# Kernel tuning notes

Hardware: AMD Instinct MI355X
Metric: run time of the kernel (lower is better)

The kernel has to match this reference:

```python
import jax, jax.numpy as jnp
import numpy as np

D_MODEL = 1024
NHEAD = 16
D_K = D_MODEL // NHEAD


def setup_inputs() -> dict:
    key = jax.random.key(0)
    ks = jax.random.split(key, 11)
    B, S = 4, 2048
    s = 1.0 / np.sqrt(D_MODEL)
    return {
        "query": jax.random.normal(ks[0], (B, S, D_MODEL), jnp.float32),
        "key": jax.random.normal(ks[1], (B, S, D_MODEL), jnp.float32),
        "value": jax.random.normal(ks[2], (B, S, D_MODEL), jnp.float32),
        "Wq": jax.random.normal(ks[3], (D_MODEL, D_MODEL), jnp.float32) * s,
        "bq": jnp.zeros((D_MODEL,), jnp.float32),
        "Wk": jax.random.normal(ks[4], (D_MODEL, D_MODEL), jnp.float32) * s,
        "bk": jnp.zeros((D_MODEL,), jnp.float32),
        "Wv": jax.random.normal(ks[5], (D_MODEL, D_MODEL), jnp.float32) * s,
        "bv": jnp.zeros((D_MODEL,), jnp.float32),
        "Wo": jax.random.normal(ks[6], (D_MODEL, D_MODEL), jnp.float32) * s,
        "bo": jnp.zeros((D_MODEL,), jnp.float32),
    }


def _split_heads(x):
    # [B, S, D] -> [B, H, S, d_k]
    B, S, _ = x.shape
    return x.reshape(B, S, NHEAD, D_K).transpose(0, 2, 1, 3)


def reference(query, key, value, Wq, bq, Wk, bk, Wv, bv, Wo, bo):
    # torch Linear: x @ W.T + b
    q = _split_heads(query @ Wq.T + bq)
    k = _split_heads(key @ Wk.T + bk)
    v = _split_heads(value @ Wv.T + bv)
    scale = 1.0 / np.sqrt(D_K).astype(np.float32)
    scores = jnp.einsum("bhqd,bhkd->bhqk", q, k) * scale
    attn = jax.nn.softmax(scores, axis=-1)  # dropout p=0 -> identity
    out = jnp.einsum("bhqk,bhkd->bhqd", attn, v)
    B, H, S, dk = out.shape
    out = out.transpose(0, 2, 1, 3).reshape(B, S, H * dk)
    return out @ Wo.T + bo
```

## Files before the change

kernel.cpp:

```cpp
#include <hip/hip_runtime.h>
#include <stdint.h>

#define DEVI static __device__ __forceinline__

typedef __attribute__((ext_vector_type(4))) float f32x4;
typedef __attribute__((ext_vector_type(16))) float f32x16;
typedef __attribute__((ext_vector_type(8))) __bf16 bf16x8;
typedef __attribute__((ext_vector_type(4))) uint16_t u16x4;
typedef uint16_t u16;

DEVI u16 f2bf(float f) {
  union { float f; uint32_t u; } v; v.f = f;
  uint32_t r = v.u + 0x7FFFu + ((v.u >> 16) & 1u);
  return (u16)(r >> 16);
}

DEVI f32x4 mfma16(bf16x8 a, bf16x8 b, f32x4 c) {
  return __builtin_amdgcn_mfma_f32_16x16x32_bf16(a, b, c, 0, 0, 0);
}

DEVI f32x16 mfma32(bf16x8 a, bf16x8 b, f32x16 c) {
  return __builtin_amdgcn_mfma_f32_32x32x16_bf16(a, b, c, 0, 0, 0);
}

DEVI void load_lds16(const void* g, void* l) {
  __builtin_amdgcn_global_load_lds(
      (const __attribute__((address_space(1))) void*)g,
      (__attribute__((address_space(3))) void*)l, 16, 0, 0);
}

DEVI bf16x8 lds_frag(const u16* p) { return *(const bf16x8*)p; }

DEVI f32x16 zero16() {
  f32x16 z;
#pragma unroll
  for (int i = 0; i < 16; ++i) z[i] = 0.f;
  return z;
}

DEVI float exp2_hw(float x) {
  float r;
  asm("v_exp_f32 %0, %1" : "=v"(r) : "v"(x));
  return r;
}

DEVI uint32_t cvtpk(float lo, float hi) {
  uint32_t r;
  asm("v_cvt_pk_bf16_f32 %0, %1, %2" : "=v"(r) : "v"(lo), "v"(hi));
  return r;
}

DEVI float max3f(float a, float b, float c) {
  float r;
  asm("v_max3_f32 %0, %1, %2, %3" : "=v"(r) : "v"(a), "v"(b), "v"(c));
  return r;
}

DEVI float partner_f(float x) { return __shfl_xor(x, 32, 64); }

DEVI void pswap_asm(uint32_t& a, uint32_t& b) {
  asm("v_permlane32_swap_b32 %0, %1" : "+v"(a), "+v"(b));
}

#define NBIG (4 * 2048 * 1024)
#define NW (1024 * 1024)

__global__ __launch_bounds__(256) void cvt_kernel(
    const float* q, const float* k, const float* v, const float* Wq,
    const float* Wk, const float* Wv, const float* Wo, u16* qb, u16* kb,
    u16* vb, u16* Wqb, u16* Wkb, u16* Wvb, u16* Wob) {
  const float* src;
  u16* dst;
  int n;
  switch (blockIdx.y) {
    case 0: src = q;  dst = qb;  n = NBIG; break;
    case 1: src = k;  dst = kb;  n = NBIG; break;
    case 2: src = v;  dst = vb;  n = NBIG; break;
    case 3: src = Wq; dst = Wqb; n = NW;   break;
    case 4: src = Wk; dst = Wkb; n = NW;   break;
    case 5: src = Wv; dst = Wvb; n = NW;   break;
    default: src = Wo; dst = Wob; n = NW;  break;
  }
  int i = (blockIdx.x * 256 + threadIdx.x) * 4;
  if (i >= n) return;
  float4 f = *(const float4*)&src[i];
  u16x4 o;
  o.x = f2bf(f.x); o.y = f2bf(f.y); o.z = f2bf(f.z); o.w = f2bf(f.w);
  *(u16x4*)&dst[i] = o;
}

DEVI void gemm_core_1024_db(const u16* __restrict__ A,
                            const u16* __restrict__ Bm, int bm, int bn,
                            u16* As, u16* Bs, f32x4 acc[4][4]) {
  const int tid = threadIdx.x;
  const int w = tid >> 6, l = tid & 63;
  const int lr = l & 15, lg = l >> 4;
  const int wr = (w >> 1) * 64, wc = (w & 1) * 64;

  for (int i = 0; i < 4; ++i)
    for (int j = 0; j < 4; ++j) acc[i][j] = (f32x4){0.f, 0.f, 0.f, 0.f};

  const int c0 = 2 * w, c1 = 2 * w + 1;
  const u16* gA0 = A + (size_t)(bm * 128 + c0 * 16 + (l >> 2)) * 1024 + (l & 3) * 8;
  const u16* gA1 = A + (size_t)(bm * 128 + c1 * 16 + (l >> 2)) * 1024 + (l & 3) * 8;
  const u16* gB0 = Bm + (size_t)(bn * 128 + c0 * 16 + (l >> 2)) * 1024 + (l & 3) * 8;
  const u16* gB1 = Bm + (size_t)(bn * 128 + c1 * 16 + (l >> 2)) * 1024 + (l & 3) * 8;
  const int sA0 = c0 * 512, sA1 = c1 * 512;

  int aoff[4], boff[4];
#pragma unroll
  for (int mi = 0; mi < 4; ++mi) aoff[mi] = (wr + mi * 16 + lr) * 32 + lg * 8;
#pragma unroll
  for (int nj = 0; nj < 4; ++nj) boff[nj] = (wc + nj * 16 + lr) * 32 + lg * 8;

  load_lds16(gA0, As + sA0);
  load_lds16(gA1, As + sA1);
  load_lds16(gB0, Bs + sA0);
  load_lds16(gB1, Bs + sA1);
  __syncthreads();

  int cur = 0;
  for (int k0 = 0; k0 < 1024; k0 += 32) {
    const int nxt = cur ^ 1;
    if (k0 + 32 < 1024) {
      load_lds16(gA0 + k0 + 32, As + nxt * 4096 + sA0);
      load_lds16(gA1 + k0 + 32, As + nxt * 4096 + sA1);
      load_lds16(gB0 + k0 + 32, Bs + nxt * 4096 + sA0);
      load_lds16(gB1 + k0 + 32, Bs + nxt * 4096 + sA1);
    }
    const u16* Ac = As + cur * 4096;
    const u16* Bc = Bs + cur * 4096;
    bf16x8 af[4], bff[4];
#pragma unroll
    for (int mi = 0; mi < 4; ++mi) af[mi] = lds_frag(&Ac[aoff[mi]]);
#pragma unroll
    for (int nj = 0; nj < 4; ++nj) bff[nj] = lds_frag(&Bc[boff[nj]]);
#pragma unroll
    for (int mi = 0; mi < 4; ++mi)
#pragma unroll
      for (int nj = 0; nj < 4; ++nj)
        acc[mi][nj] = mfma16(af[mi], bff[nj], acc[mi][nj]);
    __syncthreads();
    cur = nxt;
  }
}

__global__ __launch_bounds__(256) void proj_kernel(
    const u16* qb, const u16* kb, const u16* vb, const u16* Wq, const u16* Wk,
    const u16* Wv, const float* bq, const float* bk, const float* bv, u16* Qp,
    u16* Kp, u16* Vt) {
  __shared__ __align__(16) u16 As[2 * 128 * 32];
  __shared__ __align__(16) u16 Bs[2 * 128 * 32];
  const int z = blockIdx.z;
  const u16* A = z == 0 ? qb : z == 1 ? kb : vb;
  const u16* W = z == 0 ? Wq : z == 1 ? Wk : Wv;
  const float* bias = z == 0 ? bq : z == 1 ? bk : bv;

  f32x4 acc[4][4];
  gemm_core_1024_db(A, W, blockIdx.x, blockIdx.y, As, Bs, acc);

  const int tid = threadIdx.x;
  const int w = tid >> 6, l = tid & 63;
  const int lr = l & 15, lg = l >> 4;
  const int wr = (w >> 1) * 64, wc = (w & 1) * 64;
  const int b = (blockIdx.x * 128) >> 11;

#pragma unroll
  for (int nj = 0; nj < 4; ++nj) {
    const int col = blockIdx.y * 128 + wc + nj * 16 + lr;
    const float bb = bias[col];
    const int h = col >> 6, d = col & 63;
#pragma unroll
    for (int mi = 0; mi < 4; ++mi) {
      const int m0 = blockIdx.x * 128 + wr + mi * 16 + lg * 4;
      const int s0 = m0 & 2047;
      if (z < 2) {
        u16* dst = (z == 0) ? Qp : Kp;
#pragma unroll
        for (int r = 0; r < 4; ++r)
          dst[(((size_t)(b * 16 + h) * 2048) + s0 + r) * 64 + d] =
              f2bf(acc[mi][nj][r] + bb);
      } else {
        u16x4 pk;
        pk.x = f2bf(acc[mi][nj][0] + bb);
        pk.y = f2bf(acc[mi][nj][1] + bb);
        pk.z = f2bf(acc[mi][nj][2] + bb);
        pk.w = f2bf(acc[mi][nj][3] + bb);
        *(u16x4*)&Vt[(((size_t)(b * 16 + h) * 64) + d) * 2048 + s0] = pk;
      }
    }
  }
}

__global__ __launch_bounds__(256) void outproj_kernel(const u16* O,
                                                      const u16* Wo,
                                                      const float* bo,
                                                      float* out) {
  __shared__ __align__(16) u16 As[2 * 128 * 32];
  __shared__ __align__(16) u16 Bs[2 * 128 * 32];
  f32x4 acc[4][4];
  gemm_core_1024_db(O, Wo, blockIdx.x, blockIdx.y, As, Bs, acc);

  const int tid = threadIdx.x;
  const int w = tid >> 6, l = tid & 63;
  const int lr = l & 15, lg = l >> 4;
  const int wr = (w >> 1) * 64, wc = (w & 1) * 64;
#pragma unroll
  for (int nj = 0; nj < 4; ++nj) {
    const int col = blockIdx.y * 128 + wc + nj * 16 + lr;
    const float bb = bo[col];
#pragma unroll
    for (int mi = 0; mi < 4; ++mi) {
      const int m0 = blockIdx.x * 128 + wr + mi * 16 + lg * 4;
#pragma unroll
      for (int r = 0; r < 4; ++r)
        out[(size_t)(m0 + r) * 1024 + col] = acc[mi][nj][r] + bb;
    }
  }
}

#define LDPK 72
#define NT 32
__global__ __launch_bounds__(512) void attn_kernel(const u16* Qp, const u16* Kp,
                                                   const u16* Vt, u16* Ob) {
  __shared__ __align__(16) u16 Kl[2][64 * LDPK];
  __shared__ __align__(16) u16 Vl[2][64 * LDPK];

  const int tid = threadIdx.x, w = tid >> 6, l = tid & 63;
  const int q = l & 31, hi = l >> 5;
  const int bh = blockIdx.y;
  const int q0 = blockIdx.x * 256 + w * 32;
  const u16* Qh = Qp + (size_t)bh * 2048 * 64;
  const u16* Kh = Kp + (size_t)bh * 2048 * 64;
  const u16* Vh = Vt + (size_t)bh * 64 * 2048;

  const float SC2 = 0.1803368801f;

  bf16x8 qf[4];
#pragma unroll
  for (int ds = 0; ds < 4; ++ds)
    qf[ds] = *(const bf16x8*)&Qh[(size_t)(q0 + q) * 64 + ds * 16 + hi * 8];

  f32x16 o0 = zero16(), o1 = zero16();
  float m = -1.0e30f, ln = 0.f;

  const int srow = tid >> 3, g0 = tid & 7;

  int koff[2][4], voff[2][4];
#pragma unroll
  for (int kb = 0; kb < 2; ++kb)
#pragma unroll
    for (int ds = 0; ds < 4; ++ds)
      koff[kb][ds] = (kb * 32 + q) * LDPK + ds * 16 + hi * 8;
#pragma unroll
  for (int db = 0; db < 2; ++db)
#pragma unroll
    for (int ks = 0; ks < 4; ++ks)
      voff[db][ks] = (db * 32 + q) * LDPK + ks * 16 + hi * 8;

  bf16x8 kv = *(const bf16x8*)&Kh[srow * 64 + g0 * 8];
  bf16x8 vv = *(const bf16x8*)&Vh[(size_t)srow * 2048 + g0 * 8];
  *(bf16x8*)&Kl[0][srow * LDPK + g0 * 8] = kv;
  *(bf16x8*)&Vl[0][srow * LDPK + g0 * 8] = vv;
  kv = *(const bf16x8*)&Kh[4096 + srow * 64 + g0 * 8];
  vv = *(const bf16x8*)&Vh[(size_t)srow * 2048 + 64 + g0 * 8];
  const u16* gk = Kh + 2 * 4096 + srow * 64 + g0 * 8;
  const u16* gv = Vh + (size_t)srow * 2048 + 2 * 64 + g0 * 8;
  __syncthreads();

  for (int kt = 0; kt < NT; ++kt) {
    const int cur = kt & 1;
    const u16* Kc = Kl[cur];
    const u16* Vc = Vl[cur];

    f32x16 c0 = zero16(), c1 = zero16();
    __builtin_amdgcn_s_setprio(1);
#pragma unroll
    for (int ds = 0; ds < 4; ++ds)
      c0 = mfma32(lds_frag(&Kc[koff[0][ds]]), qf[ds], c0);
#pragma unroll
    for (int ds = 0; ds < 4; ++ds)
      c1 = mfma32(lds_frag(&Kc[koff[1][ds]]), qf[ds], c1);
    __builtin_amdgcn_s_setprio(0);

    float tm[16];
#pragma unroll
    for (int r = 0; r < 16; ++r) tm[r] = fmaxf(c0[r], c1[r]);
    {
      const float m0_ = max3f(tm[0], tm[1], tm[2]);
      const float m1_ = max3f(tm[3], tm[4], tm[5]);
      const float m2_ = max3f(tm[6], tm[7], tm[8]);
      const float m3_ = max3f(tm[9], tm[10], tm[11]);
      const float m4_ = max3f(tm[12], tm[13], tm[14]);
      const float a_ = max3f(m0_, m1_, m2_);
      const float b_ = max3f(m3_, m4_, tm[15]);
      tm[0] = fmaxf(a_, b_);
    }
    const float mx = fmaxf(tm[0], partner_f(tm[0]));
    if (!__all(mx - m <= 64.0f)) {
      const float mnew = fmaxf(m, mx);
      const float a = exp2_hw((m - mnew) * SC2);
      m = mnew;
#pragma unroll
      for (int r = 0; r < 16; ++r) { o0[r] *= a; o1[r] *= a; }
      ln *= a;
    }
    const float m2 = m * SC2;
    float p0[16], p1[16];
#pragma unroll
    for (int r = 0; r < 16; ++r) {
      p0[r] = exp2_hw(__builtin_fmaf(c0[r], SC2, -m2));
      p1[r] = exp2_hw(__builtin_fmaf(c1[r], SC2, -m2));
    }
    float ts[16];
#pragma unroll
    for (int r = 0; r < 16; ++r) ts[r] = p0[r] + p1[r];
#pragma unroll
    for (int s = 8; s > 0; s >>= 1)
#pragma unroll
      for (int r = 0; r < s; ++r) ts[r] += ts[r + s];
    ln += ts[0] + partner_f(ts[0]);

    if (kt + 1 < NT) {
      *(bf16x8*)&Kl[cur ^ 1][srow * LDPK + g0 * 8] = kv;
      *(bf16x8*)&Vl[cur ^ 1][srow * LDPK + g0 * 8] = vv;
    }
    if (kt + 2 < NT) {
      kv = *(const bf16x8*)gk;
      vv = *(const bf16x8*)gv;
      gk += 4096; gv += 64;
    }

    uint32_t wv[16];
#pragma unroll
    for (int i = 0; i < 8; ++i) {
      wv[i]     = cvtpk(p0[2 * i], p0[2 * i + 1]);
      wv[8 + i] = cvtpk(p1[2 * i], p1[2 * i + 1]);
    }
    bf16x8 pa[4];
#pragma unroll
    for (int ks = 0; ks < 4; ++ks) {
      const int base = (ks >> 1) * 8 + 4 * (ks & 1);
      uint32_t x0 = wv[base],     y0 = wv[base + 2];
      uint32_t x1 = wv[base + 1], y1 = wv[base + 3];
      pswap_asm(x0, y0);
      pswap_asm(x1, y1);
      union { uint32_t u[4]; bf16x8 v; } cvt;
      cvt.u[0] = x0; cvt.u[1] = x1; cvt.u[2] = y0; cvt.u[3] = y1;
      pa[ks] = cvt.v;
    }

    __builtin_amdgcn_s_setprio(1);
#pragma unroll
    for (int ks = 0; ks < 4; ++ks)
      o0 = mfma32(lds_frag(&Vc[voff[0][ks]]), pa[ks], o0);
#pragma unroll
    for (int ks = 0; ks < 4; ++ks)
      o1 = mfma32(lds_frag(&Vc[voff[1][ks]]), pa[ks], o1);
    __builtin_amdgcn_s_setprio(0);

    __syncthreads();
  }

  const int b2 = bh >> 4, h = bh & 15;
  const float inv = 1.0f / ln;
  u16* orow = Ob + ((size_t)(b2 * 2048 + q0 + q)) * 1024 + h * 64;
#pragma unroll
  for (int g = 0; g < 4; ++g) {
    u16x4 pk;
    pk.x = f2bf(o0[4 * g + 0] * inv);
    pk.y = f2bf(o0[4 * g + 1] * inv);
    pk.z = f2bf(o0[4 * g + 2] * inv);
    pk.w = f2bf(o0[4 * g + 3] * inv);
    *(u16x4*)&orow[8 * g + 4 * hi] = pk;
  }
#pragma unroll
  for (int g = 0; g < 4; ++g) {
    u16x4 pk;
    pk.x = f2bf(o1[4 * g + 0] * inv);
    pk.y = f2bf(o1[4 * g + 1] * inv);
    pk.z = f2bf(o1[4 * g + 2] * inv);
    pk.w = f2bf(o1[4 * g + 3] * inv);
    *(u16x4*)&orow[32 + 8 * g + 4 * hi] = pk;
  }
}

extern "C" void kernel_launch(void* const* d_in, const int* in_sizes, int n_in,
                              void* d_out, int out_size, void* d_ws,
                              size_t ws_size, hipStream_t stream) {
  const float* q  = (const float*)d_in[0];
  const float* k  = (const float*)d_in[1];
  const float* v  = (const float*)d_in[2];
  const float* Wq = (const float*)d_in[3];
  const float* bq = (const float*)d_in[4];
  const float* Wk = (const float*)d_in[5];
  const float* bk = (const float*)d_in[6];
  const float* Wv = (const float*)d_in[7];
  const float* bv = (const float*)d_in[8];
  const float* Wo = (const float*)d_in[9];
  const float* bo = (const float*)d_in[10];
  float* out = (float*)d_out;

  u16* ws = (u16*)d_ws;
  u16* qb  = ws;
  u16* kb  = qb + NBIG;
  u16* vb  = kb + NBIG;
  u16* Wqb = vb + NBIG;
  u16* Wkb = Wqb + NW;
  u16* Wvb = Wkb + NW;
  u16* Wob = Wvb + NW;
  u16* Qp  = Wob + NW;
  u16* Kp  = Qp + NBIG;
  u16* Vt  = Kp + NBIG;
  u16* O   = qb;

  cvt_kernel<<<dim3(8192, 7, 1), 256, 0, stream>>>(q, k, v, Wq, Wk, Wv, Wo, qb,
                                                   kb, vb, Wqb, Wkb, Wvb, Wob);
  proj_kernel<<<dim3(64, 8, 3), 256, 0, stream>>>(qb, kb, vb, Wqb, Wkb, Wvb,
                                                  bq, bk, bv, Qp, Kp, Vt);
  attn_kernel<<<dim3(8, 64, 1), 512, 0, stream>>>(Qp, Kp, Vt, O);
  outproj_kernel<<<dim3(64, 8, 1), 256, 0, stream>>>(O, Wob, bo, out);
}
```

Baseline: 226.3 us.

## Use three-stage LDS pipeline with vmcnt waits in projection GEMM core

Replaces the double-buffered GEMM mainloop with a triple-buffered one that keeps two K-tiles of global-to-LDS loads in flight. It waits with s_waitcnt vmcnt(4) plus a raw s_barrier instead of __syncthreads, so the wave waits only for the oldest stage rather than draining all loads. This is meant to hide global load latency behind MFMA work in the projection and output-projection GEMMs. The cost is 50% more LDS per block, which may lower occupancy, and it relies on the exact vmcnt accounting of the load_lds16 instructions being correct.

```diff
diff --git a/kernel.cpp b/kernel.cpp
--- a/kernel.cpp
+++ b/kernel.cpp
@@ -61,6 +61,9 @@
 DEVI void pswap_asm(uint32_t& a, uint32_t& b) {
   asm("v_permlane32_swap_b32 %0, %1" : "+v"(a), "+v"(b));
 }
+
+DEVI void wait_vm4() { asm volatile("s_waitcnt vmcnt(4)" ::: "memory"); }
+DEVI void wait_vm0() { asm volatile("s_waitcnt vmcnt(0)" ::: "memory"); }
 
 #define NBIG (4 * 2048 * 1024)
 #define NW (1024 * 1024)
@@ -89,7 +92,7 @@
   *(u16x4*)&dst[i] = o;
 }
 
-DEVI void gemm_core_1024_db(const u16* __restrict__ A,
+DEVI void gemm_core_1024_p2(const u16* __restrict__ A,
                             const u16* __restrict__ Bm, int bm, int bn,
                             u16* As, u16* Bs, f32x4 acc[4][4]) {
   const int tid = threadIdx.x;
@@ -117,16 +120,25 @@
   load_lds16(gA1, As + sA1);
   load_lds16(gB0, Bs + sA0);
   load_lds16(gB1, Bs + sA1);
-  __syncthreads();
+  load_lds16(gA0 + 32, As + 4096 + sA0);
+  load_lds16(gA1 + 32, As + 4096 + sA1);
+  load_lds16(gB0 + 32, Bs + 4096 + sA0);
+  load_lds16(gB1 + 32, Bs + 4096 + sA1);
+  wait_vm4();
+  __builtin_amdgcn_sched_barrier(0);
+  __builtin_amdgcn_s_barrier();
 
   int cur = 0;
-  for (int k0 = 0; k0 < 1024; k0 += 32) {
-    const int nxt = cur ^ 1;
-    if (k0 + 32 < 1024) {
-      load_lds16(gA0 + k0 + 32, As + nxt * 4096 + sA0);
-      load_lds16(gA1 + k0 + 32, As + nxt * 4096 + sA1);
-      load_lds16(gB0 + k0 + 32, Bs + nxt * 4096 + sA0);
-      load_lds16(gB1 + k0 + 32, Bs + nxt * 4096 + sA1);
+  for (int t = 0; t < 32; ++t) {
+    if (t + 2 < 32) {
+      const int st = cur >= 1 ? cur - 1 : 2;
+      const int ko = (t + 2) * 32;
+      u16* Ab = As + st * 4096;
+      u16* Bb = Bs + st * 4096;
+      load_lds16(gA0 + ko, Ab + sA0);
+      load_lds16(gA1 + ko, Ab + sA1);
+      load_lds16(gB0 + ko, Bb + sA0);
+      load_lds16(gB1 + ko, Bb + sA1);
     }
     const u16* Ac = As + cur * 4096;
     const u16* Bc = Bs + cur * 4096;
@@ -140,8 +152,16 @@
 #pragma unroll
       for (int nj = 0; nj < 4; ++nj)
         acc[mi][nj] = mfma16(af[mi], bff[nj], acc[mi][nj]);
-    __syncthreads();
-    cur = nxt;
+    if (t + 2 < 32) {
+      wait_vm4();
+      __builtin_amdgcn_sched_barrier(0);
+      __builtin_amdgcn_s_barrier();
+    } else if (t + 1 < 32) {
+      wait_vm0();
+      __builtin_amdgcn_sched_barrier(0);
+      __builtin_amdgcn_s_barrier();
+    }
+    cur = cur == 2 ? 0 : cur + 1;
   }
 }
 
@@ -149,15 +169,15 @@
     const u16* qb, const u16* kb, const u16* vb, const u16* Wq, const u16* Wk,
     const u16* Wv, const float* bq, const float* bk, const float* bv, u16* Qp,
     u16* Kp, u16* Vt) {
-  __shared__ __align__(16) u16 As[2 * 128 * 32];
-  __shared__ __align__(16) u16 Bs[2 * 128 * 32];
+  __shared__ __align__(16) u16 As[3 * 128 * 32];
+  __shared__ __align__(16) u16 Bs[3 * 128 * 32];
   const int z = blockIdx.z;
   const u16* A = z == 0 ? qb : z == 1 ? kb : vb;
   const u16* W = z == 0 ? Wq : z == 1 ? Wk : Wv;
   const float* bias = z == 0 ? bq : z == 1 ? bk : bv;
 
   f32x4 acc[4][4];
-  gemm_core_1024_db(A, W, blockIdx.x, blockIdx.y, As, Bs, acc);
+  gemm_core_1024_p2(A, W, blockIdx.x, blockIdx.y, As, Bs, acc);
 
   const int tid = threadIdx.x;
   const int w = tid >> 6, l = tid & 63;
@@ -196,10 +216,10 @@
                                                       const u16* Wo,
                                                       const float* bo,
                                                       float* out) {
-  __shared__ __align__(16) u16 As[2 * 128 * 32];
-  __shared__ __align__(16) u16 Bs[2 * 128 * 32];
+  __shared__ __align__(16) u16 As[3 * 128 * 32];
+  __shared__ __align__(16) u16 Bs[3 * 128 * 32];
   f32x4 acc[4][4];
-  gemm_core_1024_db(O, Wo, blockIdx.x, blockIdx.y, As, Bs, acc);
+  gemm_core_1024_p2(O, Wo, blockIdx.x, blockIdx.y, As, Bs, acc);
 
   const int tid = threadIdx.x;
   const int w = tid >> 6, l = tid & 63;
```

Measured after the change: 240.9 us. +6.5%, slower.

## Rewrite QKV projection GEMM with 256x256 tiles, 512 threads, swizzled LDS pipeline

Applied to the files above, without the earlier changes.

Replaces the 128x128 projection GEMM with a 256x256-tile kernel using 8 waves, each computing 128x64. It uses K-step 64, XOR-swizzled LDS layout, and double-buffered direct-to-LDS loads staggered across four sub-phases with explicit waitcnt/barriers and setprio around MFMA bursts. This aims to raise arithmetic intensity and overlap global loads with MFMA. The trade-offs are a 384-block grid that may underfill waves on 256 CUs, higher register and LDS use, and fragile hand-tuned synchronization.

```diff
diff --git a/kernel.cpp b/kernel.cpp
--- a/kernel.cpp
+++ b/kernel.cpp
@@ -89,6 +89,149 @@
   *(u16x4*)&dst[i] = o;
 }
 
+__global__ __launch_bounds__(512) void proj_kernel(
+    const u16* qb, const u16* kb, const u16* vb, const u16* Wq, const u16* Wk,
+    const u16* Wv, const float* bq, const float* bk, const float* bv, u16* Qp,
+    u16* Kp, u16* Vt) {
+  __shared__ __align__(16) u16 As[2][2][8192];
+  __shared__ __align__(16) u16 Bs[2][2][8192];
+
+  const int z = blockIdx.z;
+  const u16* A = z == 0 ? qb : z == 1 ? kb : vb;
+  const u16* W = z == 0 ? Wq : z == 1 ? Wk : Wv;
+  const float* bias = z == 0 ? bq : z == 1 ? bk : bv;
+
+  const int tid = threadIdx.x, w = tid >> 6, l = tid & 63;
+  const int lr = l & 15, lg = l >> 4;
+  const int wm = w >> 2, wn = w & 3;
+  const int bm = blockIdx.x, bn = blockIdx.y;
+
+  const int r0 = tid >> 3;
+  const int jg = (tid & 7) ^ (r0 & 7);
+  const int r1 = r0 + 64;
+  const u16* gA0 = A + (size_t)(bm * 256 + r0) * 1024 + jg * 8;
+  const u16* gA1 = A + (size_t)(bm * 256 + r1) * 1024 + jg * 8;
+  const u16* gB0 = W + (size_t)(bn * 256 + r0) * 1024 + jg * 8;
+  const u16* gB1 = W + (size_t)(bn * 256 + r1) * 1024 + jg * 8;
+  const int ls0 = w * 512;
+  const int ls1 = 4096 + w * 512;
+
+  auto stB = [&](int dd, int h, int kt) {
+    load_lds16(gB0 + (size_t)h * 128 * 1024 + kt * 64, &Bs[dd][h][ls0]);
+    load_lds16(gB1 + (size_t)h * 128 * 1024 + kt * 64, &Bs[dd][h][ls1]);
+  };
+  auto stA_s0 = [&](int dd, int kt) {
+    load_lds16(gA0 + kt * 64, &As[dd][0][ls0]);
+    load_lds16(gA0 + (size_t)128 * 1024 + kt * 64, &As[dd][1][ls0]);
+  };
+  auto stA_s1 = [&](int dd, int kt) {
+    load_lds16(gA1 + kt * 64, &As[dd][0][ls1]);
+    load_lds16(gA1 + (size_t)128 * 1024 + kt * 64, &As[dd][1][ls1]);
+  };
+
+  int aoff[8][2], boff[4][2];
+#pragma unroll
+  for (int mi = 0; mi < 8; ++mi)
+#pragma unroll
+    for (int ks = 0; ks < 2; ++ks)
+      aoff[mi][ks] = (mi * 16 + lr) * 64 + (((ks * 4 + lg) ^ (lr & 7)) * 8);
+#pragma unroll
+  for (int nf = 0; nf < 4; ++nf)
+#pragma unroll
+    for (int ks = 0; ks < 2; ++ks)
+      boff[nf][ks] =
+          ((wn & 1) * 64 + nf * 16 + lr) * 64 + (((ks * 4 + lg) ^ (lr & 7)) * 8);
+
+  f32x4 acc[8][4];
+#pragma unroll
+  for (int i = 0; i < 8; ++i)
+#pragma unroll
+    for (int j = 0; j < 4; ++j) acc[i][j] = (f32x4){0.f, 0.f, 0.f, 0.f};
+
+  stB(0, 0, 0);
+  stB(0, 1, 0);
+  stA_s0(0, 0);
+  stA_s1(0, 0);
+  asm volatile("s_waitcnt vmcnt(2)" ::: "memory");
+  __builtin_amdgcn_sched_barrier(0);
+  __builtin_amdgcn_s_barrier();
+
+  for (int t = 0; t < 16; ++t) {
+    const int d = t & 1;
+    const u16* Aw = &As[d][wm][0];
+    const u16* Bw = &Bs[d][wn >> 1][0];
+    bf16x8 bf[4][2];
+#pragma unroll
+    for (int q = 0; q < 4; ++q) {
+      if (q == 0) {
+#pragma unroll
+        for (int nf = 0; nf < 4; ++nf)
+#pragma unroll
+          for (int ks = 0; ks < 2; ++ks)
+            bf[nf][ks] = lds_frag(&Bw[boff[nf][ks]]);
+      }
+      bf16x8 af[2][2];
+#pragma unroll
+      for (int j = 0; j < 2; ++j)
+#pragma unroll
+        for (int ks = 0; ks < 2; ++ks)
+          af[j][ks] = lds_frag(&Aw[aoff[2 * q + j][ks]]);
+      if (t + 1 < 16) {
+        if (q == 0) stB(d ^ 1, 0, t + 1);
+        else if (q == 1) stB(d ^ 1, 1, t + 1);
+        else if (q == 2) stA_s0(d ^ 1, t + 1);
+        else stA_s1(d ^ 1, t + 1);
+      }
+      __builtin_amdgcn_s_barrier();
+      asm volatile("s_waitcnt lgkmcnt(0)" ::: "memory");
+      __builtin_amdgcn_sched_barrier(0);
+      __builtin_amdgcn_s_setprio(1);
+#pragma unroll
+      for (int j = 0; j < 2; ++j)
+#pragma unroll
+        for (int ks = 0; ks < 2; ++ks)
+#pragma unroll
+          for (int nf = 0; nf < 4; ++nf)
+            acc[2 * q + j][nf] = mfma16(af[j][ks], bf[nf][ks], acc[2 * q + j][nf]);
+      __builtin_amdgcn_s_setprio(0);
+      if (q == 1) {
+        if (t < 15) asm volatile("s_waitcnt vmcnt(4)" ::: "memory");
+        else        asm volatile("s_waitcnt vmcnt(0)" ::: "memory");
+      } else if (q == 3 && t < 15) {
+        asm volatile("s_waitcnt vmcnt(2)" ::: "memory");
+      }
+      __builtin_amdgcn_s_barrier();
+    }
+  }
+
+  const int b = (bm * 256) >> 11;
+#pragma unroll
+  for (int nj = 0; nj < 4; ++nj) {
+    const int col = bn * 256 + wn * 64 + nj * 16 + lr;
+    const float bb = bias[col];
+    const int h = col >> 6, dd = col & 63;
+#pragma unroll
+    for (int mi = 0; mi < 8; ++mi) {
+      const int m0 = bm * 256 + wm * 128 + mi * 16 + lg * 4;
+      const int s0 = m0 & 2047;
+      if (z < 2) {
+        u16* dst = (z == 0) ? Qp : Kp;
+#pragma unroll
+        for (int r = 0; r < 4; ++r)
+          dst[(((size_t)(b * 16 + h) * 2048) + s0 + r) * 64 + dd] =
+              f2bf(acc[mi][nj][r] + bb);
+      } else {
+        u16x4 pk;
+        pk.x = f2bf(acc[mi][nj][0] + bb);
+        pk.y = f2bf(acc[mi][nj][1] + bb);
+        pk.z = f2bf(acc[mi][nj][2] + bb);
+        pk.w = f2bf(acc[mi][nj][3] + bb);
+        *(u16x4*)&Vt[(((size_t)(b * 16 + h) * 64) + dd) * 2048 + s0] = pk;
+      }
+    }
+  }
+}
+
 DEVI void gemm_core_1024_db(const u16* __restrict__ A,
                             const u16* __restrict__ Bm, int bm, int bn,
                             u16* As, u16* Bs, f32x4 acc[4][4]) {
@@ -142,53 +285,6 @@
         acc[mi][nj] = mfma16(af[mi], bff[nj], acc[mi][nj]);
     __syncthreads();
     cur = nxt;
-  }
-}
-
-__global__ __launch_bounds__(256) void proj_kernel(
-    const u16* qb, const u16* kb, const u16* vb, const u16* Wq, const u16* Wk,
-    const u16* Wv, const float* bq, const float* bk, const float* bv, u16* Qp,
-    u16* Kp, u16* Vt) {
-  __shared__ __align__(16) u16 As[2 * 128 * 32];
-  __shared__ __align__(16) u16 Bs[2 * 128 * 32];
-  const int z = blockIdx.z;
-  const u16* A = z == 0 ? qb : z == 1 ? kb : vb;
-  const u16* W = z == 0 ? Wq : z == 1 ? Wk : Wv;
-  const float* bias = z == 0 ? bq : z == 1 ? bk : bv;
-
-  f32x4 acc[4][4];
-  gemm_core_1024_db(A, W, blockIdx.x, blockIdx.y, As, Bs, acc);
-
-  const int tid = threadIdx.x;
-  const int w = tid >> 6, l = tid & 63;
-  const int lr = l & 15, lg = l >> 4;
-  const int wr = (w >> 1) * 64, wc = (w & 1) * 64;
-  const int b = (blockIdx.x * 128) >> 11;
-
-#pragma unroll
-  for (int nj = 0; nj < 4; ++nj) {
-    const int col = blockIdx.y * 128 + wc + nj * 16 + lr;
-    const float bb = bias[col];
-    const int h = col >> 6, d = col & 63;
-#pragma unroll
-    for (int mi = 0; mi < 4; ++mi) {
-      const int m0 = blockIdx.x * 128 + wr + mi * 16 + lg * 4;
-      const int s0 = m0 & 2047;
-      if (z < 2) {
-        u16* dst = (z == 0) ? Qp : Kp;
-#pragma unroll
-        for (int r = 0; r < 4; ++r)
-          dst[(((size_t)(b * 16 + h) * 2048) + s0 + r) * 64 + d] =
-              f2bf(acc[mi][nj][r] + bb);
-      } else {
-        u16x4 pk;
-        pk.x = f2bf(acc[mi][nj][0] + bb);
-        pk.y = f2bf(acc[mi][nj][1] + bb);
-        pk.z = f2bf(acc[mi][nj][2] + bb);
-        pk.w = f2bf(acc[mi][nj][3] + bb);
-        *(u16x4*)&Vt[(((size_t)(b * 16 + h) * 64) + d) * 2048 + s0] = pk;
-      }
-    }
   }
 }
 
@@ -416,7 +512,7 @@
 
   cvt_kernel<<<dim3(8192, 7, 1), 256, 0, stream>>>(q, k, v, Wq, Wk, Wv, Wo, qb,
                                                    kb, vb, Wqb, Wkb, Wvb, Wob);
-  proj_kernel<<<dim3(64, 8, 3), 256, 0, stream>>>(qb, kb, vb, Wqb, Wkb, Wvb,
+  proj_kernel<<<dim3(32, 4, 3), 512, 0, stream>>>(qb, kb, vb, Wqb, Wkb, Wvb,
                                                   bq, bk, bv, Qp, Kp, Vt);
   attn_kernel<<<dim3(8, 64, 1), 512, 0, stream>>>(Qp, Kp, Vt, O);
   outproj_kernel<<<dim3(64, 8, 1), 256, 0, stream>>>(O, Wob, bo, out);
```

Result: no change. 226.0 us (-0.1%).

## Fuse fp32-to-bf16 activation conversion into projection GEMM A-tile loads

Applied to the files above, without the earlier changes.

The separate conversion pass over the q/k/v activations is removed. The projection kernel now streams fp32 activations straight into LDS through an XOR-swizzled layout and converts them to bf16 in registers before the MFMA. This avoids writing and re-reading about 50 MB of bf16 intermediates and drops most of the conversion kernel's work. In exchange the A tile takes twice the LDS space and global traffic per tile, and every tile is converted again for each of the 8 column blocks.

```diff
diff --git a/kernel.cpp b/kernel.cpp
--- a/kernel.cpp
+++ b/kernel.cpp
@@ -50,6 +50,15 @@
   return r;
 }
 
+DEVI bf16x8 cvt8v(f32x4 lo, f32x4 hi) {
+  union { uint32_t u[4]; bf16x8 v; } c;
+  c.u[0] = cvtpk(lo[0], lo[1]);
+  c.u[1] = cvtpk(lo[2], lo[3]);
+  c.u[2] = cvtpk(hi[0], hi[1]);
+  c.u[3] = cvtpk(hi[2], hi[3]);
+  return c.v;
+}
+
 DEVI float max3f(float a, float b, float c) {
   float r;
   asm("v_max3_f32 %0, %1, %2, %3" : "=v"(r) : "v"(a), "v"(b), "v"(c));
@@ -65,74 +74,102 @@
 #define NBIG (4 * 2048 * 1024)
 #define NW (1024 * 1024)
 
-__global__ __launch_bounds__(256) void cvt_kernel(
-    const float* q, const float* k, const float* v, const float* Wq,
-    const float* Wk, const float* Wv, const float* Wo, u16* qb, u16* kb,
-    u16* vb, u16* Wqb, u16* Wkb, u16* Wvb, u16* Wob) {
+__global__ __launch_bounds__(256) void cvt_kernel(const float* Wq,
+                                                  const float* Wk,
+                                                  const float* Wv,
+                                                  const float* Wo, u16* Wqb,
+                                                  u16* Wkb, u16* Wvb,
+                                                  u16* Wob) {
   const float* src;
   u16* dst;
-  int n;
   switch (blockIdx.y) {
-    case 0: src = q;  dst = qb;  n = NBIG; break;
-    case 1: src = k;  dst = kb;  n = NBIG; break;
-    case 2: src = v;  dst = vb;  n = NBIG; break;
-    case 3: src = Wq; dst = Wqb; n = NW;   break;
-    case 4: src = Wk; dst = Wkb; n = NW;   break;
-    case 5: src = Wv; dst = Wvb; n = NW;   break;
-    default: src = Wo; dst = Wob; n = NW;  break;
+    case 0: src = Wq; dst = Wqb; break;
+    case 1: src = Wk; dst = Wkb; break;
+    case 2: src = Wv; dst = Wvb; break;
+    default: src = Wo; dst = Wob; break;
   }
   int i = (blockIdx.x * 256 + threadIdx.x) * 4;
-  if (i >= n) return;
+  if (i >= NW) return;
   float4 f = *(const float4*)&src[i];
   u16x4 o;
   o.x = f2bf(f.x); o.y = f2bf(f.y); o.z = f2bf(f.z); o.w = f2bf(f.w);
   *(u16x4*)&dst[i] = o;
 }
 
-DEVI void gemm_core_1024_db(const u16* __restrict__ A,
-                            const u16* __restrict__ Bm, int bm, int bn,
-                            u16* As, u16* Bs, f32x4 acc[4][4]) {
+__global__ __launch_bounds__(256) void proj_kernel(
+    const float* qx, const float* kx, const float* vx, const u16* Wq,
+    const u16* Wk, const u16* Wv, const float* bq, const float* bk,
+    const float* bv, u16* Qp, u16* Kp, u16* Vt) {
+  __shared__ __align__(16) float Af[2][128 * 32];
+  __shared__ __align__(16) u16 Bs[2][128 * 32];
+
+  const int z = blockIdx.z;
+  const float* A32 = z == 0 ? qx : z == 1 ? kx : vx;
+  const u16* W = z == 0 ? Wq : z == 1 ? Wk : Wv;
+  const float* bias = z == 0 ? bq : z == 1 ? bk : bv;
+  const int bm = blockIdx.x, bn = blockIdx.y;
+
   const int tid = threadIdx.x;
   const int w = tid >> 6, l = tid & 63;
   const int lr = l & 15, lg = l >> 4;
   const int wr = (w >> 1) * 64, wc = (w & 1) * 64;
 
+  const int ar = l >> 3;
+  const int aj = (l & 7) ^ ar;
+  const float* gA[4];
+  int laoff[4];
+#pragma unroll
+  for (int i = 0; i < 4; ++i) {
+    const int c = 4 * w + i;
+    gA[i] = A32 + (size_t)(bm * 128 + c * 8 + ar) * 1024 + aj * 4;
+    laoff[i] = c * 256;
+  }
+  const int c0 = 2 * w, c1 = 2 * w + 1;
+  const u16* gB0 = W + (size_t)(bn * 128 + c0 * 16 + (l >> 2)) * 1024 + (l & 3) * 8;
+  const u16* gB1 = W + (size_t)(bn * 128 + c1 * 16 + (l >> 2)) * 1024 + (l & 3) * 8;
+  const int sb0 = c0 * 512, sb1 = c1 * 512;
+
+  int aoff0[4], aoff1[4], boff[4];
+#pragma unroll
+  for (int mi = 0; mi < 4; ++mi) {
+    const int row = wr + mi * 16 + lr;
+    aoff0[mi] = row * 32 + (((lg * 2)     ) ^ (row & 7)) * 4;
+    aoff1[mi] = row * 32 + (((lg * 2) + 1) ^ (row & 7)) * 4;
+  }
+#pragma unroll
+  for (int nj = 0; nj < 4; ++nj) boff[nj] = (wc + nj * 16 + lr) * 32 + lg * 8;
+
+  f32x4 acc[4][4];
+#pragma unroll
   for (int i = 0; i < 4; ++i)
+#pragma unroll
     for (int j = 0; j < 4; ++j) acc[i][j] = (f32x4){0.f, 0.f, 0.f, 0.f};
 
-  const int c0 = 2 * w, c1 = 2 * w + 1;
-  const u16* gA0 = A + (size_t)(bm * 128 + c0 * 16 + (l >> 2)) * 1024 + (l & 3) * 8;
-  const u16* gA1 = A + (size_t)(bm * 128 + c1 * 16 + (l >> 2)) * 1024 + (l & 3) * 8;
-  const u16* gB0 = Bm + (size_t)(bn * 128 + c0 * 16 + (l >> 2)) * 1024 + (l & 3) * 8;
-  const u16* gB1 = Bm + (size_t)(bn * 128 + c1 * 16 + (l >> 2)) * 1024 + (l & 3) * 8;
-  const int sA0 = c0 * 512, sA1 = c1 * 512;
-
-  int aoff[4], boff[4];
-#pragma unroll
-  for (int mi = 0; mi < 4; ++mi) aoff[mi] = (wr + mi * 16 + lr) * 32 + lg * 8;
-#pragma unroll
-  for (int nj = 0; nj < 4; ++nj) boff[nj] = (wc + nj * 16 + lr) * 32 + lg * 8;
-
-  load_lds16(gA0, As + sA0);
-  load_lds16(gA1, As + sA1);
-  load_lds16(gB0, Bs + sA0);
-  load_lds16(gB1, Bs + sA1);
+#pragma unroll
+  for (int i = 0; i < 4; ++i) load_lds16(gA[i], &Af[0][laoff[i]]);
+  load_lds16(gB0, &Bs[0][sb0]);
+  load_lds16(gB1, &Bs[0][sb1]);
   __syncthreads();
 
   int cur = 0;
   for (int k0 = 0; k0 < 1024; k0 += 32) {
     const int nxt = cur ^ 1;
     if (k0 + 32 < 1024) {
-      load_lds16(gA0 + k0 + 32, As + nxt * 4096 + sA0);
-      load_lds16(gA1 + k0 + 32, As + nxt * 4096 + sA1);
-      load_lds16(gB0 + k0 + 32, Bs + nxt * 4096 + sA0);
-      load_lds16(gB1 + k0 + 32, Bs + nxt * 4096 + sA1);
-    }
-    const u16* Ac = As + cur * 4096;
-    const u16* Bc = Bs + cur * 4096;
+#pragma unroll
+      for (int i = 0; i < 4; ++i)
+        load_lds16(gA[i] + k0 + 32, &Af[nxt][laoff[i]]);
+      load_lds16(gB0 + k0 + 32, &Bs[nxt][sb0]);
+      load_lds16(gB1 + k0 + 32, &Bs[nxt][sb1]);
+    }
+    const float* Ac = Af[cur];
+    const u16* Bc = Bs[cur];
     bf16x8 af[4], bff[4];
 #pragma unroll
-    for (int mi = 0; mi < 4; ++mi) af[mi] = lds_frag(&Ac[aoff[mi]]);
+    for (int mi = 0; mi < 4; ++mi) {
+      const f32x4 lo = *(const f32x4*)&Ac[aoff0[mi]];
+      const f32x4 hi = *(const f32x4*)&Ac[aoff1[mi]];
+      af[mi] = cvt8v(lo, hi);
+    }
 #pragma unroll
     for (int nj = 0; nj < 4; ++nj) bff[nj] = lds_frag(&Bc[boff[nj]]);
 #pragma unroll
@@ -143,36 +180,16 @@
     __syncthreads();
     cur = nxt;
   }
-}
-
-__global__ __launch_bounds__(256) void proj_kernel(
-    const u16* qb, const u16* kb, const u16* vb, const u16* Wq, const u16* Wk,
-    const u16* Wv, const float* bq, const float* bk, const float* bv, u16* Qp,
-    u16* Kp, u16* Vt) {
-  __shared__ __align__(16) u16 As[2 * 128 * 32];
-  __shared__ __align__(16) u16 Bs[2 * 128 * 32];
-  const int z = blockIdx.z;
-  const u16* A = z == 0 ? qb : z == 1 ? kb : vb;
-  const u16* W = z == 0 ? Wq : z == 1 ? Wk : Wv;
-  const float* bias = z == 0 ? bq : z == 1 ? bk : bv;
-
-  f32x4 acc[4][4];
-  gemm_core_1024_db(A, W, blockIdx.x, blockIdx.y, As, Bs, acc);
-
-  const int tid = threadIdx.x;
-  const int w = tid >> 6, l = tid & 63;
-  const int lr = l & 15, lg = l >> 4;
-  const int wr = (w >> 1) * 64, wc = (w & 1) * 64;
+
   const int b = (blockIdx.x * 128) >> 11;
-
 #pragma unroll
   for (int nj = 0; nj < 4; ++nj) {
-    const int col = blockIdx.y * 128 + wc + nj * 16 + lr;
+    const int col = bn * 128 + wc + nj * 16 + lr;
     const float bb = bias[col];
     const int h = col >> 6, d = col & 63;
 #pragma unroll
     for (int mi = 0; mi < 4; ++mi) {
-      const int m0 = blockIdx.x * 128 + wr + mi * 16 + lg * 4;
+      const int m0 = bm * 128 + wr + mi * 16 + lg * 4;
       const int s0 = m0 & 2047;
       if (z < 2) {
         u16* dst = (z == 0) ? Qp : Kp;
@@ -189,6 +206,62 @@
         *(u16x4*)&Vt[(((size_t)(b * 16 + h) * 64) + d) * 2048 + s0] = pk;
       }
     }
+  }
+}
+
+DEVI void gemm_core_1024_db(const u16* __restrict__ A,
+                            const u16* __restrict__ Bm, int bm, int bn,
+                            u16* As, u16* Bs, f32x4 acc[4][4]) {
+  const int tid = threadIdx.x;
+  const int w = tid >> 6, l = tid & 63;
+  const int lr = l & 15, lg = l >> 4;
+  const int wr = (w >> 1) * 64, wc = (w & 1) * 64;
+
+  for (int i = 0; i < 4; ++i)
+    for (int j = 0; j < 4; ++j) acc[i][j] = (f32x4){0.f, 0.f, 0.f, 0.f};
+
+  const int c0 = 2 * w, c1 = 2 * w + 1;
+  const u16* gA0 = A + (size_t)(bm * 128 + c0 * 16 + (l >> 2)) * 1024 + (l & 3) * 8;
+  const u16* gA1 = A + (size_t)(bm * 128 + c1 * 16 + (l >> 2)) * 1024 + (l & 3) * 8;
+  const u16* gB0 = Bm + (size_t)(bn * 128 + c0 * 16 + (l >> 2)) * 1024 + (l & 3) * 8;
+  const u16* gB1 = Bm + (size_t)(bn * 128 + c1 * 16 + (l >> 2)) * 1024 + (l & 3) * 8;
+  const int sA0 = c0 * 512, sA1 = c1 * 512;
+
+  int aoff[4], boff[4];
+#pragma unroll
+  for (int mi = 0; mi < 4; ++mi) aoff[mi] = (wr + mi * 16 + lr) * 32 + lg * 8;
+#pragma unroll
+  for (int nj = 0; nj < 4; ++nj) boff[nj] = (wc + nj * 16 + lr) * 32 + lg * 8;
+
+  load_lds16(gA0, As + sA0);
+  load_lds16(gA1, As + sA1);
+  load_lds16(gB0, Bs + sA0);
+  load_lds16(gB1, Bs + sA1);
+  __syncthreads();
+
+  int cur = 0;
+  for (int k0 = 0; k0 < 1024; k0 += 32) {
+    const int nxt = cur ^ 1;
+    if (k0 + 32 < 1024) {
+      load_lds16(gA0 + k0 + 32, As + nxt * 4096 + sA0);
+      load_lds16(gA1 + k0 + 32, As + nxt * 4096 + sA1);
+      load_lds16(gB0 + k0 + 32, Bs + nxt * 4096 + sA0);
+      load_lds16(gB1 + k0 + 32, Bs + nxt * 4096 + sA1);
+    }
+    const u16* Ac = As + cur * 4096;
+    const u16* Bc = Bs + cur * 4096;
+    bf16x8 af[4], bff[4];
+#pragma unroll
+    for (int mi = 0; mi < 4; ++mi) af[mi] = lds_frag(&Ac[aoff[mi]]);
+#pragma unroll
+    for (int nj = 0; nj < 4; ++nj) bff[nj] = lds_frag(&Bc[boff[nj]]);
+#pragma unroll
+    for (int mi = 0; mi < 4; ++mi)
+#pragma unroll
+      for (int nj = 0; nj < 4; ++nj)
+        acc[mi][nj] = mfma16(af[mi], bff[nj], acc[mi][nj]);
+    __syncthreads();
+    cur = nxt;
   }
 }
 
@@ -402,22 +475,19 @@
   float* out = (float*)d_out;
 
   u16* ws = (u16*)d_ws;
-  u16* qb  = ws;
-  u16* kb  = qb + NBIG;
-  u16* vb  = kb + NBIG;
-  u16* Wqb = vb + NBIG;
+  u16* Wqb = ws;
   u16* Wkb = Wqb + NW;
   u16* Wvb = Wkb + NW;
   u16* Wob = Wvb + NW;
   u16* Qp  = Wob + NW;
   u16* Kp  = Qp + NBIG;
   u16* Vt  = Kp + NBIG;
-  u16* O   = qb;
-
-  cvt_kernel<<<dim3(8192, 7, 1), 256, 0, stream>>>(q, k, v, Wq, Wk, Wv, Wo, qb,
-                                                   kb, vb, Wqb, Wkb, Wvb, Wob);
-  proj_kernel<<<dim3(64, 8, 3), 256, 0, stream>>>(qb, kb, vb, Wqb, Wkb, Wvb,
-                                                  bq, bk, bv, Qp, Kp, Vt);
+  u16* O   = Vt + NBIG;
+
+  cvt_kernel<<<dim3(1024, 4, 1), 256, 0, stream>>>(Wq, Wk, Wv, Wo, Wqb, Wkb,
+                                                   Wvb, Wob);
+  proj_kernel<<<dim3(64, 8, 3), 256, 0, stream>>>(q, k, v, Wqb, Wkb, Wvb, bq,
+                                                  bk, bv, Qp, Kp, Vt);
   attn_kernel<<<dim3(8, 64, 1), 512, 0, stream>>>(Qp, Kp, Vt, O);
   outproj_kernel<<<dim3(64, 8, 1), 256, 0, stream>>>(O, Wob, bo, out);
 }
```

New measurement: 223.6 us. No clear change (-1.2%).
